# Performance work log

Measured on AMD Instinct MI355X. Metric: run time of the kernel, lower is better.

The kernel has to match this reference:

```python
import jax, jax.numpy as jnp
import numpy as np

D = 1  # dilation


def _unfold3x3(x, d):
    # x: [B, C, H, W] -> [B, H*W, 9, C]; matches torch.nn.Unfold(kernel_size=3,
    # dilation=d, padding=d, stride=1) followed by the module's reshapes.
    B, C, H, W = x.shape
    xp = jnp.pad(x, ((0, 0), (0, 0), (d, d), (d, d)))
    pats = [xp[:, :, i * d:i * d + H, j * d:j * d + W] for i in range(3) for j in range(3)]
    p = jnp.stack(pats, axis=0)  # [9, B, C, H, W], kernel positions row-major (center = 4)
    return p.transpose(1, 3, 4, 0, 2).reshape(B, H * W, 9, C)


def _masked_bn(h, m, gamma, beta, eps=1e-5):
    # BatchNorm1d in training mode applied only to rows selected by bool mask m
    # (the torch code gathers rows, BNs them, scatters back into zeros).
    # Stats are the biased mean/var over the selected rows, per channel.
    axes = tuple(range(h.ndim - 1))
    mf = m[..., None].astype(h.dtype)
    n = jnp.maximum(mf.sum(), 1.0)
    mean = (h * mf).sum(axes) / n
    var = (((h - mean) ** 2 * mf)).sum(axes) / n
    return (h - mean) * jax.lax.rsqrt(var + eps) * gamma + beta


def setup_inputs() -> dict:
    key = jax.random.key(0)
    ks = jax.random.split(key, 8)
    B, H, W = 2, 64, 1024
    Cin, Cout, Cm = 64, 64, 4
    s = 0.1
    x = jax.random.normal(ks[0], (B, Cm + Cin, H, W), jnp.float32)
    mask = (jax.random.uniform(ks[1], (B, 1, H, W)) > 0.3).astype(jnp.float32)
    return {
        "x": x,
        "mask": mask,
        "w1": jax.random.normal(ks[2], (8, Cm), jnp.float32) * s,
        "bn1_g": jnp.ones(8, jnp.float32),
        "bn1_b": jnp.zeros(8, jnp.float32),
        "w2": jax.random.normal(ks[3], (1, 8), jnp.float32) * s,
        "b2": jnp.zeros(1, jnp.float32),
        "g1": jax.random.normal(ks[4], (8, Cm), jnp.float32) * s,
        "gbn1_g": jnp.ones(8, jnp.float32),
        "gbn1_b": jnp.zeros(8, jnp.float32),
        "g2": jax.random.normal(ks[5], (8, 8), jnp.float32) * s,
        "gbn2_g": jnp.ones(8, jnp.float32),
        "gbn2_b": jnp.zeros(8, jnp.float32),
        "w_agg": jax.random.normal(ks[6], (Cout, 72 + Cin), jnp.float32) * s,
        "abn_g": jnp.ones(Cout, jnp.float32),
        "abn_b": jnp.zeros(Cout, jnp.float32),
    }


def reference(x, mask, w1, bn1_g, bn1_b, w2, b2, g1, gbn1_g, gbn1_b, g2, gbn2_g, gbn2_b, w_agg, abn_g, abn_b):
    B, C, H, W = x.shape
    xu = _unfold3x3(x, D)                      # [B, HW, 9, C]
    mu = _unfold3x3(mask, D)[..., 0]           # [B, HW, 9]
    msel = mu > 0                              # valid-neighbor mask
    mp0 = msel[:, :, 4]                        # valid-center mask [B, HW]
    pn = xu[..., :4] - xu[:, :, 4:5, :4]       # relative meta coords [B, HW, 9, 4]
    feats = xu[..., 4:]                        # neighbor features [B, HW, 9, Cin]

    # weight branch (dense compute + mask == torch's gather/scatter)
    h = _masked_bn(pn @ w1.T, msel, bn1_g, bn1_b)
    h = jax.nn.relu(h) @ w2.T + b2             # [B, HW, 9, 1]
    wts = jnp.where(msel, h[..., 0], 0.0)      # zeros at invalid neighbors pre-softmax
    wts = jax.nn.softmax(wts, axis=-1)[..., None]

    fagg = (wts * feats).sum(axis=2)           # [B, HW, Cin]

    # geo branch
    g = jax.nn.relu(_masked_bn(pn @ g1.T, msel, gbn1_g, gbn1_b))
    g = jax.nn.relu(_masked_bn(g @ g2.T, msel, gbn2_g, gbn2_b))
    g = jnp.where(msel[..., None], g, 0.0)
    g = (wts * g).reshape(B, H * W, 72)

    # aggregation over valid centers
    out = jnp.concatenate([fagg, g], axis=-1) @ w_agg.T
    out = jax.nn.relu(_masked_bn(out, mp0, abn_g, abn_b))
    out = jnp.where(mp0[..., None], out, 0.0)  # [B, HW, Cout]
    return out.transpose(0, 2, 1).reshape(B, -1, H, W)  # fold with k=1 == reshape
```

## Files before the change

### kernel.cpp

```cpp
#include <hip/hip_runtime.h>

#define HW_ 65536
#define W_ 1024
#define H_ 64
#define B_ 2
#define C_ 68
#define NPIX 131072
#define EPS 1e-5f

typedef __attribute__((ext_vector_type(8))) short short8;
typedef __attribute__((ext_vector_type(4))) float floatx4;

__device__ __forceinline__ unsigned short f2bf(float f) {
  unsigned u = __float_as_uint(f);
  u += 0x7fffu + ((u >> 16) & 1u);
  return (unsigned short)(u >> 16);
}
__device__ __forceinline__ unsigned pack2(float a, float b) {
  return (unsigned)f2bf(a) | ((unsigned)f2bf(b) << 16);
}
__device__ __forceinline__ float wred(float v) {
  v += __shfl_xor(v, 1);  v += __shfl_xor(v, 2);  v += __shfl_xor(v, 4);
  v += __shfl_xor(v, 8);  v += __shfl_xor(v, 16); v += __shfl_xor(v, 32);
  return v;
}
__device__ __forceinline__ int swz_tile(int bid) {
  return (bid & 7) * 64 + (bid >> 3);
}

__global__ __launch_bounds__(256) void k_stats1(
    const float* __restrict__ x, const float* __restrict__ mask,
    const float* __restrict__ w1, const float* __restrict__ g1,
    float* __restrict__ ws) {
  float acc[34];
#pragma unroll
  for (int i = 0; i < 34; i++) acc[i] = 0.f;

  int p = swz_tile(blockIdx.x) * 256 + threadIdx.x;
  {
    int b = p >> 16, s = p & (HW_ - 1);
    int h = s >> 10, w = s & (W_ - 1);
    const float* xb = x + (size_t)b * C_ * HW_;
    const float* mb = mask + (size_t)b * HW_;
    float xc0 = xb[s], xc1 = xb[HW_ + s], xc2 = xb[2 * HW_ + s], xc3 = xb[3 * HW_ + s];
    acc[33] += (mb[s] > 0.f) ? 1.f : 0.f;
#pragma unroll
    for (int k = 0; k < 9; k++) {
      int di = k / 3 - 1, dj = k % 3 - 1;
      int hh = h + di, ww = w + dj;
      bool inb = ((unsigned)hh < (unsigned)H_) && ((unsigned)ww < (unsigned)W_);
      int ns = hh * W_ + ww;
      float mval = inb ? mb[ns] : 0.f;
      if (mval > 0.f) {
        float pn0 = xb[ns] - xc0;
        float pn1 = xb[HW_ + ns] - xc1;
        float pn2 = xb[2 * HW_ + ns] - xc2;
        float pn3 = xb[3 * HW_ + ns] - xc3;
        acc[32] += 1.f;
#pragma unroll
        for (int o = 0; o < 8; o++) {
          float ta = pn0 * w1[o * 4] + pn1 * w1[o * 4 + 1] + pn2 * w1[o * 4 + 2] + pn3 * w1[o * 4 + 3];
          acc[o] += ta; acc[8 + o] += ta * ta;
          float tg = pn0 * g1[o * 4] + pn1 * g1[o * 4 + 1] + pn2 * g1[o * 4 + 2] + pn3 * g1[o * 4 + 3];
          acc[16 + o] += tg; acc[24 + o] += tg * tg;
        }
      }
    }
  }
  __shared__ float red[4][34];
  int lane = threadIdx.x & 63, wave = threadIdx.x >> 6;
#pragma unroll
  for (int i = 0; i < 34; i++) {
    float r = wred(acc[i]);
    if (lane == 0) red[wave][i] = r;
  }
  __syncthreads();
  if (threadIdx.x < 34)
    atomicAdd(&ws[threadIdx.x],
              red[0][threadIdx.x] + red[1][threadIdx.x] + red[2][threadIdx.x] + red[3][threadIdx.x]);
}

__global__ __launch_bounds__(256) void k_stats2(
    const float* __restrict__ x, const float* __restrict__ mask,
    const float* __restrict__ g1, const float* __restrict__ gbn1_g,
    const float* __restrict__ gbn1_b, const float* __restrict__ g2,
    float* __restrict__ ws) {
  __shared__ float sc[8], sh[8];
  if (threadIdx.x < 8) {
    int o = threadIdx.x;
    float n = fmaxf(ws[32], 1.f);
    float mean = ws[16 + o] / n;
    float var = ws[24 + o] / n - mean * mean;
    float s = gbn1_g[o] * rsqrtf(var + EPS);
    sc[o] = s; sh[o] = gbn1_b[o] - mean * s;
  }
  __syncthreads();

  float acc[16];
#pragma unroll
  for (int i = 0; i < 16; i++) acc[i] = 0.f;

  int p = swz_tile(blockIdx.x) * 256 + threadIdx.x;
  {
    int b = p >> 16, s = p & (HW_ - 1);
    int h = s >> 10, w = s & (W_ - 1);
    const float* xb = x + (size_t)b * C_ * HW_;
    const float* mb = mask + (size_t)b * HW_;
    float xc0 = xb[s], xc1 = xb[HW_ + s], xc2 = xb[2 * HW_ + s], xc3 = xb[3 * HW_ + s];
#pragma unroll
    for (int k = 0; k < 9; k++) {
      int di = k / 3 - 1, dj = k % 3 - 1;
      int hh = h + di, ww = w + dj;
      bool inb = ((unsigned)hh < (unsigned)H_) && ((unsigned)ww < (unsigned)W_);
      int ns = hh * W_ + ww;
      float mval = inb ? mb[ns] : 0.f;
      if (mval > 0.f) {
        float pn0 = xb[ns] - xc0;
        float pn1 = xb[HW_ + ns] - xc1;
        float pn2 = xb[2 * HW_ + ns] - xc2;
        float pn3 = xb[3 * HW_ + ns] - xc3;
        float gb[8];
#pragma unroll
        for (int o = 0; o < 8; o++) {
          float tg = pn0 * g1[o * 4] + pn1 * g1[o * 4 + 1] + pn2 * g1[o * 4 + 2] + pn3 * g1[o * 4 + 3];
          gb[o] = fmaxf(sc[o] * tg + sh[o], 0.f);
        }
#pragma unroll
        for (int j = 0; j < 8; j++) {
          float t2 = 0.f;
#pragma unroll
          for (int o = 0; o < 8; o++) t2 += gb[o] * g2[j * 8 + o];
          acc[j] += t2; acc[8 + j] += t2 * t2;
        }
      }
    }
  }
  __shared__ float red[4][16];
  int lane = threadIdx.x & 63, wave = threadIdx.x >> 6;
#pragma unroll
  for (int i = 0; i < 16; i++) {
    float r = wred(acc[i]);
    if (lane == 0) red[wave][i] = r;
  }
  __syncthreads();
  if (threadIdx.x < 16)
    atomicAdd(&ws[40 + threadIdx.x],
              red[0][threadIdx.x] + red[1][threadIdx.x] + red[2][threadIdx.x] + red[3][threadIdx.x]);
}

__global__ __launch_bounds__(256) void k_fused(
    const float* __restrict__ x, const float* __restrict__ mask,
    const float* __restrict__ w1, const float* __restrict__ bn1_g,
    const float* __restrict__ bn1_b, const float* __restrict__ w2,
    const float* __restrict__ b2, const float* __restrict__ g1,
    const float* __restrict__ gbn1_g, const float* __restrict__ gbn1_b,
    const float* __restrict__ g2, const float* __restrict__ gbn2_g,
    const float* __restrict__ gbn2_b, const float* __restrict__ w_agg,
    const float* __restrict__ ws, float* __restrict__ out_pre,
    float* __restrict__ wsum) {
  __shared__ uint4 vecA[17][256];
  __shared__ float sA[8], hA[8], sG1[8], hG1[8], sG2[8], hG2[8];

  if (threadIdx.x < 24) {
    int o = threadIdx.x & 7;
    float n = fmaxf(ws[32], 1.f);
    float sum, sum2, gma, bta;
    if (threadIdx.x < 8)       { sum = ws[o];      sum2 = ws[8 + o];  gma = bn1_g[o];  bta = bn1_b[o]; }
    else if (threadIdx.x < 16) { sum = ws[16 + o]; sum2 = ws[24 + o]; gma = gbn1_g[o]; bta = gbn1_b[o]; }
    else                       { sum = ws[40 + o]; sum2 = ws[48 + o]; gma = gbn2_g[o]; bta = gbn2_b[o]; }
    float mean = sum / n, var = sum2 / n - mean * mean;
    float s = gma * rsqrtf(var + EPS);
    float sft = bta - mean * s;
    if (threadIdx.x < 8)       { sA[o] = s;  hA[o] = sft; }
    else if (threadIdx.x < 16) { sG1[o] = s; hG1[o] = sft; }
    else                       { sG2[o] = s; hG2[o] = sft; }
  }
  __syncthreads();

  int tile = swz_tile(blockIdx.x);
  int p0 = tile * 256;
  int p = p0 + threadIdx.x;
  int b = p >> 16, s = p & (HW_ - 1);
  int h = s >> 10, w = s & (W_ - 1);
  const float* xb = x + (size_t)b * C_ * HW_;
  const float* mb = mask + (size_t)b * HW_;
  float xc0 = xb[s], xc1 = xb[HW_ + s], xc2 = xb[2 * HW_ + s], xc3 = xb[3 * HW_ + s];
  float b2v = b2[0];

  float ev[9]; int nsv[9]; bool inbv[9], mselv[9];
  float mx = -1e30f;
#pragma unroll
  for (int k = 0; k < 9; k++) {
    int di = k / 3 - 1, dj = k % 3 - 1;
    int hh = h + di, ww = w + dj;
    bool inb = ((unsigned)hh < (unsigned)H_) && ((unsigned)ww < (unsigned)W_);
    int ns = hh * W_ + ww;
    inbv[k] = inb; nsv[k] = ns;
    float mval = inb ? mb[ns] : 0.f;
    bool msel = mval > 0.f;
    mselv[k] = msel;
    float wp = 0.f;
    if (msel) {
      float pn0 = xb[ns] - xc0;
      float pn1 = xb[HW_ + ns] - xc1;
      float pn2 = xb[2 * HW_ + ns] - xc2;
      float pn3 = xb[3 * HW_ + ns] - xc3;
      float accw = 0.f;
#pragma unroll
      for (int o = 0; o < 8; o++) {
        float ta = pn0 * w1[o * 4] + pn1 * w1[o * 4 + 1] + pn2 * w1[o * 4 + 2] + pn3 * w1[o * 4 + 3];
        accw += fmaxf(sA[o] * ta + hA[o], 0.f) * w2[o];
      }
      wp = accw + b2v;
    }
    ev[k] = wp;
    mx = fmaxf(mx, wp);
  }
  float den = 0.f;
#pragma unroll
  for (int k = 0; k < 9; k++) { ev[k] = __expf(ev[k] - mx); den += ev[k]; }
  float inv = 1.f / den;

  float fagg[64];
#pragma unroll
  for (int c = 0; c < 64; c++) fagg[c] = 0.f;

#pragma unroll
  for (int k = 0; k < 9; k++) {
    float wt = ev[k] * inv;
    int ns = nsv[k];
    uint4 pk; pk.x = pk.y = pk.z = pk.w = 0u;
    if (mselv[k]) {
      float pn0 = xb[ns] - xc0;
      float pn1 = xb[HW_ + ns] - xc1;
      float pn2 = xb[2 * HW_ + ns] - xc2;
      float pn3 = xb[3 * HW_ + ns] - xc3;
      float gb[8];
#pragma unroll
      for (int o = 0; o < 8; o++) {
        float tg = pn0 * g1[o * 4] + pn1 * g1[o * 4 + 1] + pn2 * g1[o * 4 + 2] + pn3 * g1[o * 4 + 3];
        gb[o] = fmaxf(sG1[o] * tg + hG1[o], 0.f);
      }
      float gv[8];
#pragma unroll
      for (int j = 0; j < 8; j++) {
        float t2 = 0.f;
#pragma unroll
        for (int o = 0; o < 8; o++) t2 += gb[o] * g2[j * 8 + o];
        float gg = fmaxf(sG2[j] * t2 + hG2[j], 0.f);
        gv[j] = wt * gg;
      }
      pk.x = pack2(gv[0], gv[1]); pk.y = pack2(gv[2], gv[3]);
      pk.z = pack2(gv[4], gv[5]); pk.w = pack2(gv[6], gv[7]);
    }
    vecA[8 + k][threadIdx.x] = pk;
    if (inbv[k]) {
      const float* xf = xb + 4 * HW_ + ns;
#pragma unroll
      for (int c = 0; c < 64; c++) fagg[c] += wt * xf[c * HW_];
    }
  }
#pragma unroll
  for (int c = 0; c < 64; c += 8) {
    uint4 pk;
    pk.x = pack2(fagg[c], fagg[c + 1]);     pk.y = pack2(fagg[c + 2], fagg[c + 3]);
    pk.z = pack2(fagg[c + 4], fagg[c + 5]); pk.w = pack2(fagg[c + 6], fagg[c + 7]);
    vecA[c >> 3][threadIdx.x] = pk;
  }
  __syncthreads();

  int lane = threadIdx.x & 63, wave = threadIdx.x >> 6;
  int q = lane >> 4, r = lane & 15;

  short8 Bf[4][5];
#pragma unroll
  for (int nt = 0; nt < 4; nt++) {
    int n = nt * 16 + r;
#pragma unroll
    for (int ks = 0; ks < 5; ks++) {
      int k0 = ks * 32 + q * 8;
      uint4 pk; pk.x = pk.y = pk.z = pk.w = 0u;
      if (k0 < 136) {
        float4 f0 = *reinterpret_cast<const float4*>(w_agg + n * 136 + k0);
        float4 f1 = *reinterpret_cast<const float4*>(w_agg + n * 136 + k0 + 4);
        pk.x = pack2(f0.x, f0.y); pk.y = pack2(f0.z, f0.w);
        pk.z = pack2(f1.x, f1.y); pk.w = pack2(f1.z, f1.w);
      }
      Bf[nt][ks] = *reinterpret_cast<short8*>(&pk);
    }
  }

  floatx4 acc[4][4];
#pragma unroll
  for (int m = 0; m < 4; m++)
#pragma unroll
    for (int nt = 0; nt < 4; nt++) acc[m][nt] = (floatx4){0.f, 0.f, 0.f, 0.f};

#pragma unroll
  for (int m = 0; m < 4; m++) {
    int mt = wave * 4 + m;
    int pix = mt * 16 + r;
    short8 Af[5];
#pragma unroll
    for (int ks = 0; ks < 5; ks++) {
      int chunk = ks * 4 + q;
      if (chunk < 17)
        Af[ks] = *reinterpret_cast<const short8*>(&vecA[chunk][pix]);
      else
        Af[ks] = (short8){0, 0, 0, 0, 0, 0, 0, 0};
    }
#pragma unroll
    for (int nt = 0; nt < 4; nt++)
#pragma unroll
      for (int ks = 0; ks < 5; ks++)
        acc[m][nt] = __builtin_amdgcn_mfma_f32_16x16x32_bf16(Af[ks], Bf[nt][ks], acc[m][nt], 0, 0, 0);
  }

  float aS[4] = {0.f, 0.f, 0.f, 0.f}, aQ[4] = {0.f, 0.f, 0.f, 0.f};
  int s0 = p0 & (HW_ - 1);
#pragma unroll
  for (int m = 0; m < 4; m++) {
    int mt = wave * 4 + m;
    int srow = s0 + mt * 16 + q * 4;
    float4 mv = *reinterpret_cast<const float4*>(mb + srow);
    float m0 = (mv.x > 0.f) ? 1.f : 0.f, m1 = (mv.y > 0.f) ? 1.f : 0.f;
    float m2 = (mv.z > 0.f) ? 1.f : 0.f, m3 = (mv.w > 0.f) ? 1.f : 0.f;
#pragma unroll
    for (int nt = 0; nt < 4; nt++) {
      int ch = nt * 16 + r;
      float4 ov;
      ov.x = acc[m][nt][0]; ov.y = acc[m][nt][1];
      ov.z = acc[m][nt][2]; ov.w = acc[m][nt][3];
      aS[nt] += ov.x * m0 + ov.y * m1 + ov.z * m2 + ov.w * m3;
      aQ[nt] += ov.x * ov.x * m0 + ov.y * ov.y * m1 + ov.z * ov.z * m2 + ov.w * ov.w * m3;
      *reinterpret_cast<float4*>(out_pre + ((size_t)(b * 64 + ch)) * HW_ + srow) = ov;
    }
  }

  __syncthreads();
  float* rS = (float*)&vecA[0][0];
  float* rQ = rS + 256;
#pragma unroll
  for (int nt = 0; nt < 4; nt++) {
    float v1 = aS[nt], v2 = aQ[nt];
    v1 += __shfl_xor(v1, 16); v1 += __shfl_xor(v1, 32);
    v2 += __shfl_xor(v2, 16); v2 += __shfl_xor(v2, 32);
    if (lane < 16) { rS[wave * 64 + nt * 16 + lane] = v1; rQ[wave * 64 + nt * 16 + lane] = v2; }
  }
  __syncthreads();
  if (threadIdx.x < 64) {
    atomicAdd(&wsum[64 + threadIdx.x],
              rS[threadIdx.x] + rS[64 + threadIdx.x] + rS[128 + threadIdx.x] + rS[192 + threadIdx.x]);
    atomicAdd(&wsum[128 + threadIdx.x],
              rQ[threadIdx.x] + rQ[64 + threadIdx.x] + rQ[128 + threadIdx.x] + rQ[192 + threadIdx.x]);
  }
}

__global__ __launch_bounds__(256) void k_final(
    const float* __restrict__ out_pre, const float* __restrict__ mask,
    const float* __restrict__ abn_g, const float* __restrict__ abn_b,
    const float* __restrict__ ws, float* __restrict__ out) {
  __shared__ float sc[64], sh[64];
  if (threadIdx.x < 64) {
    int c = threadIdx.x;
    float n0 = fmaxf(ws[33], 1.f);
    float mean = ws[64 + c] / n0;
    float var = ws[128 + c] / n0 - mean * mean;
    float s = abn_g[c] * rsqrtf(var + EPS);
    sc[c] = s; sh[c] = abn_b[c] - mean * s;
  }
  __syncthreads();
  int i4 = (blockIdx.x * 256 + threadIdx.x) * 4;
  if (i4 >= B_ * 64 * HW_) return;
  int c = (i4 >> 16) & 63;
  int b = i4 >> 22;
  int s = i4 & (HW_ - 1);
  float4 v = *reinterpret_cast<const float4*>(out_pre + i4);
  float4 m = *reinterpret_cast<const float4*>(mask + (size_t)b * HW_ + s);
  float4 o;
  o.x = (m.x > 0.f) ? fmaxf(v.x * sc[c] + sh[c], 0.f) : 0.f;
  o.y = (m.y > 0.f) ? fmaxf(v.y * sc[c] + sh[c], 0.f) : 0.f;
  o.z = (m.z > 0.f) ? fmaxf(v.z * sc[c] + sh[c], 0.f) : 0.f;
  o.w = (m.w > 0.f) ? fmaxf(v.w * sc[c] + sh[c], 0.f) : 0.f;
  *reinterpret_cast<float4*>(out + i4) = o;
}

extern "C" void kernel_launch(void* const* d_in, const int* in_sizes, int n_in,
                              void* d_out, int out_size, void* d_ws, size_t ws_size,
                              hipStream_t stream) {
  const float* x      = (const float*)d_in[0];
  const float* mask   = (const float*)d_in[1];
  const float* w1     = (const float*)d_in[2];
  const float* bn1_g  = (const float*)d_in[3];
  const float* bn1_b  = (const float*)d_in[4];
  const float* w2     = (const float*)d_in[5];
  const float* b2     = (const float*)d_in[6];
  const float* g1     = (const float*)d_in[7];
  const float* gbn1_g = (const float*)d_in[8];
  const float* gbn1_b = (const float*)d_in[9];
  const float* g2     = (const float*)d_in[10];
  const float* gbn2_g = (const float*)d_in[11];
  const float* gbn2_b = (const float*)d_in[12];
  const float* w_agg  = (const float*)d_in[13];
  const float* abn_g  = (const float*)d_in[14];
  const float* abn_b  = (const float*)d_in[15];
  float* out = (float*)d_out;

  size_t need = 1024 + (size_t)NPIX * 64 * 4;
  if (ws_size < need) return;

  float* wsf = (float*)d_ws;
  float* out_pre = (float*)((char*)d_ws + 1024);

  hipMemsetAsync(d_ws, 0, 1024, stream);
  k_stats1<<<512, 256, 0, stream>>>(x, mask, w1, g1, wsf);
  k_stats2<<<512, 256, 0, stream>>>(x, mask, g1, gbn1_g, gbn1_b, g2, wsf);
  k_fused<<<512, 256, 0, stream>>>(x, mask, w1, bn1_g, bn1_b, w2, b2, g1,
                                   gbn1_g, gbn1_b, g2, gbn2_g, gbn2_b, w_agg,
                                   wsf, out_pre, wsf);
  k_final<<<8192, 256, 0, stream>>>(out_pre, mask, abn_g, abn_b, wsf, out);
}
```

Before: 224.5 us.

## Fuse all stages into one persistent kernel with software grid barriers

Merges the two statistics kernels, the fused compute kernel and the final BN kernel into a single 512-block launch that synchronises BatchNorm statistics through atomic-counter grid barriers. Neighbor meta deltas are kept in registers across phases, and the final BN/ReLU is applied straight from the MFMA accumulators. This drops the 32 MB out_pre intermediate write and re-read plus three extra launches. It relies on all 512 blocks being co-resident (launch_bounds 256,2 on 256 CUs). The barrier gives up after a spin cap, which could silently yield wrong statistics, and the larger live register state may cause spills.

```diff
diff --git a/kernel.cpp b/kernel.cpp
--- a/kernel.cpp
+++ b/kernel.cpp
@@ -6,6 +6,7 @@
 #define B_ 2
 #define C_ 68
 #define NPIX 131072
+#define NBLK 512
 #define EPS 1e-5f
 
 typedef __attribute__((ext_vector_type(8))) short short8;
@@ -27,128 +28,33 @@
 __device__ __forceinline__ int swz_tile(int bid) {
   return (bid & 7) * 64 + (bid >> 3);
 }
-
-__global__ __launch_bounds__(256) void k_stats1(
-    const float* __restrict__ x, const float* __restrict__ mask,
-    const float* __restrict__ w1, const float* __restrict__ g1,
-    float* __restrict__ ws) {
-  float acc[34];
-#pragma unroll
-  for (int i = 0; i < 34; i++) acc[i] = 0.f;
-
-  int p = swz_tile(blockIdx.x) * 256 + threadIdx.x;
-  {
-    int b = p >> 16, s = p & (HW_ - 1);
-    int h = s >> 10, w = s & (W_ - 1);
-    const float* xb = x + (size_t)b * C_ * HW_;
-    const float* mb = mask + (size_t)b * HW_;
-    float xc0 = xb[s], xc1 = xb[HW_ + s], xc2 = xb[2 * HW_ + s], xc3 = xb[3 * HW_ + s];
-    acc[33] += (mb[s] > 0.f) ? 1.f : 0.f;
-#pragma unroll
-    for (int k = 0; k < 9; k++) {
-      int di = k / 3 - 1, dj = k % 3 - 1;
-      int hh = h + di, ww = w + dj;
-      bool inb = ((unsigned)hh < (unsigned)H_) && ((unsigned)ww < (unsigned)W_);
-      int ns = hh * W_ + ww;
-      float mval = inb ? mb[ns] : 0.f;
-      if (mval > 0.f) {
-        float pn0 = xb[ns] - xc0;
-        float pn1 = xb[HW_ + ns] - xc1;
-        float pn2 = xb[2 * HW_ + ns] - xc2;
-        float pn3 = xb[3 * HW_ + ns] - xc3;
-        acc[32] += 1.f;
-#pragma unroll
-        for (int o = 0; o < 8; o++) {
-          float ta = pn0 * w1[o * 4] + pn1 * w1[o * 4 + 1] + pn2 * w1[o * 4 + 2] + pn3 * w1[o * 4 + 3];
-          acc[o] += ta; acc[8 + o] += ta * ta;
-          float tg = pn0 * g1[o * 4] + pn1 * g1[o * 4 + 1] + pn2 * g1[o * 4 + 2] + pn3 * g1[o * 4 + 3];
-          acc[16 + o] += tg; acc[24 + o] += tg * tg;
-        }
-      }
-    }
-  }
-  __shared__ float red[4][34];
-  int lane = threadIdx.x & 63, wave = threadIdx.x >> 6;
-#pragma unroll
-  for (int i = 0; i < 34; i++) {
-    float r = wred(acc[i]);
-    if (lane == 0) red[wave][i] = r;
-  }
-  __syncthreads();
-  if (threadIdx.x < 34)
-    atomicAdd(&ws[threadIdx.x],
-              red[0][threadIdx.x] + red[1][threadIdx.x] + red[2][threadIdx.x] + red[3][threadIdx.x]);
-}
-
-__global__ __launch_bounds__(256) void k_stats2(
-    const float* __restrict__ x, const float* __restrict__ mask,
-    const float* __restrict__ g1, const float* __restrict__ gbn1_g,
-    const float* __restrict__ gbn1_b, const float* __restrict__ g2,
-    float* __restrict__ ws) {
-  __shared__ float sc[8], sh[8];
-  if (threadIdx.x < 8) {
-    int o = threadIdx.x;
-    float n = fmaxf(ws[32], 1.f);
-    float mean = ws[16 + o] / n;
-    float var = ws[24 + o] / n - mean * mean;
-    float s = gbn1_g[o] * rsqrtf(var + EPS);
-    sc[o] = s; sh[o] = gbn1_b[o] - mean * s;
-  }
-  __syncthreads();
-
-  float acc[16];
-#pragma unroll
-  for (int i = 0; i < 16; i++) acc[i] = 0.f;
-
-  int p = swz_tile(blockIdx.x) * 256 + threadIdx.x;
-  {
-    int b = p >> 16, s = p & (HW_ - 1);
-    int h = s >> 10, w = s & (W_ - 1);
-    const float* xb = x + (size_t)b * C_ * HW_;
-    const float* mb = mask + (size_t)b * HW_;
-    float xc0 = xb[s], xc1 = xb[HW_ + s], xc2 = xb[2 * HW_ + s], xc3 = xb[3 * HW_ + s];
-#pragma unroll
-    for (int k = 0; k < 9; k++) {
-      int di = k / 3 - 1, dj = k % 3 - 1;
-      int hh = h + di, ww = w + dj;
-      bool inb = ((unsigned)hh < (unsigned)H_) && ((unsigned)ww < (unsigned)W_);
-      int ns = hh * W_ + ww;
-      float mval = inb ? mb[ns] : 0.f;
-      if (mval > 0.f) {
-        float pn0 = xb[ns] - xc0;
-        float pn1 = xb[HW_ + ns] - xc1;
-        float pn2 = xb[2 * HW_ + ns] - xc2;
-        float pn3 = xb[3 * HW_ + ns] - xc3;
-        float gb[8];
-#pragma unroll
-        for (int o = 0; o < 8; o++) {
-          float tg = pn0 * g1[o * 4] + pn1 * g1[o * 4 + 1] + pn2 * g1[o * 4 + 2] + pn3 * g1[o * 4 + 3];
-          gb[o] = fmaxf(sc[o] * tg + sh[o], 0.f);
-        }
-#pragma unroll
-        for (int j = 0; j < 8; j++) {
-          float t2 = 0.f;
-#pragma unroll
-          for (int o = 0; o < 8; o++) t2 += gb[o] * g2[j * 8 + o];
-          acc[j] += t2; acc[8 + j] += t2 * t2;
-        }
-      }
-    }
-  }
-  __shared__ float red[4][16];
-  int lane = threadIdx.x & 63, wave = threadIdx.x >> 6;
-#pragma unroll
-  for (int i = 0; i < 16; i++) {
-    float r = wred(acc[i]);
-    if (lane == 0) red[wave][i] = r;
-  }
-  __syncthreads();
-  if (threadIdx.x < 16)
-    atomicAdd(&ws[40 + threadIdx.x],
-              red[0][threadIdx.x] + red[1][threadIdx.x] + red[2][threadIdx.x] + red[3][threadIdx.x]);
-}
-
-__global__ __launch_bounds__(256) void k_fused(
+__device__ __forceinline__ float wsld(const float* p) {
+  return __hip_atomic_load(p, __ATOMIC_RELAXED, __HIP_MEMORY_SCOPE_AGENT);
+}
+
+__device__ __forceinline__ void gridbar(unsigned* bar) {
+  __syncthreads();
+  if (threadIdx.x == 0) {
+    __threadfence();
+    unsigned gen = __hip_atomic_load(&bar[1], __ATOMIC_RELAXED, __HIP_MEMORY_SCOPE_AGENT);
+    unsigned arrived =
+        __hip_atomic_fetch_add(&bar[0], 1u, __ATOMIC_ACQ_REL, __HIP_MEMORY_SCOPE_AGENT);
+    if (arrived == NBLK - 1) {
+      __hip_atomic_store(&bar[0], 0u, __ATOMIC_RELAXED, __HIP_MEMORY_SCOPE_AGENT);
+      __hip_atomic_store(&bar[1], gen + 1u, __ATOMIC_RELEASE, __HIP_MEMORY_SCOPE_AGENT);
+    } else {
+      long long spins = 0;
+      while (__hip_atomic_load(&bar[1], __ATOMIC_ACQUIRE, __HIP_MEMORY_SCOPE_AGENT) == gen) {
+        if (++spins > (1LL << 22)) break;
+        __builtin_amdgcn_s_sleep(8);
+      }
+    }
+    __threadfence();
+  }
+  __syncthreads();
+}
+
+__global__ __launch_bounds__(256, 2) void k_all(
     const float* __restrict__ x, const float* __restrict__ mask,
     const float* __restrict__ w1, const float* __restrict__ bn1_g,
     const float* __restrict__ bn1_b, const float* __restrict__ w2,
@@ -156,59 +62,152 @@
     const float* __restrict__ gbn1_g, const float* __restrict__ gbn1_b,
     const float* __restrict__ g2, const float* __restrict__ gbn2_g,
     const float* __restrict__ gbn2_b, const float* __restrict__ w_agg,
-    const float* __restrict__ ws, float* __restrict__ out_pre,
-    float* __restrict__ wsum) {
+    const float* __restrict__ abn_g, const float* __restrict__ abn_b,
+    float* __restrict__ ws, float* __restrict__ out) {
+  unsigned* bar = (unsigned*)(ws + 248);
+
   __shared__ uint4 vecA[17][256];
+  __shared__ float red[4][34];
   __shared__ float sA[8], hA[8], sG1[8], hG1[8], sG2[8], hG2[8];
-
-  if (threadIdx.x < 24) {
-    int o = threadIdx.x & 7;
-    float n = fmaxf(ws[32], 1.f);
-    float sum, sum2, gma, bta;
-    if (threadIdx.x < 8)       { sum = ws[o];      sum2 = ws[8 + o];  gma = bn1_g[o];  bta = bn1_b[o]; }
-    else if (threadIdx.x < 16) { sum = ws[16 + o]; sum2 = ws[24 + o]; gma = gbn1_g[o]; bta = gbn1_b[o]; }
-    else                       { sum = ws[40 + o]; sum2 = ws[48 + o]; gma = gbn2_g[o]; bta = gbn2_b[o]; }
-    float mean = sum / n, var = sum2 / n - mean * mean;
-    float s = gma * rsqrtf(var + EPS);
-    float sft = bta - mean * s;
-    if (threadIdx.x < 8)       { sA[o] = s;  hA[o] = sft; }
-    else if (threadIdx.x < 16) { sG1[o] = s; hG1[o] = sft; }
-    else                       { sG2[o] = s; hG2[o] = sft; }
-  }
-  __syncthreads();
+  __shared__ float scD[64], shD[64];
 
   int tile = swz_tile(blockIdx.x);
   int p0 = tile * 256;
-  int p = p0 + threadIdx.x;
+  int p = p0 + (int)threadIdx.x;
   int b = p >> 16, s = p & (HW_ - 1);
   int h = s >> 10, w = s & (W_ - 1);
   const float* xb = x + (size_t)b * C_ * HW_;
   const float* mb = mask + (size_t)b * HW_;
+  int lane = threadIdx.x & 63, wave = threadIdx.x >> 6;
+  int q = lane >> 4, r = lane & 15;
+
   float xc0 = xb[s], xc1 = xb[HW_ + s], xc2 = xb[2 * HW_ + s], xc3 = xb[3 * HW_ + s];
-  float b2v = b2[0];
-
-  float ev[9]; int nsv[9]; bool inbv[9], mselv[9];
-  float mx = -1e30f;
+
+  float pn[9][4];
+  int nsv[9];
+  unsigned mbits = 0u, ibits = 0u;
+  float cntk = 0.f;
 #pragma unroll
   for (int k = 0; k < 9; k++) {
     int di = k / 3 - 1, dj = k % 3 - 1;
     int hh = h + di, ww = w + dj;
     bool inb = ((unsigned)hh < (unsigned)H_) && ((unsigned)ww < (unsigned)W_);
     int ns = hh * W_ + ww;
-    inbv[k] = inb; nsv[k] = ns;
+    nsv[k] = ns;
+    pn[k][0] = 0.f; pn[k][1] = 0.f; pn[k][2] = 0.f; pn[k][3] = 0.f;
+    if (inb) ibits |= (1u << k);
     float mval = inb ? mb[ns] : 0.f;
-    bool msel = mval > 0.f;
-    mselv[k] = msel;
+    if (mval > 0.f) {
+      mbits |= (1u << k);
+      cntk += 1.f;
+      pn[k][0] = xb[ns] - xc0;
+      pn[k][1] = xb[HW_ + ns] - xc1;
+      pn[k][2] = xb[2 * HW_ + ns] - xc2;
+      pn[k][3] = xb[3 * HW_ + ns] - xc3;
+    }
+  }
+
+  {
+    float acc[34];
+#pragma unroll
+    for (int i = 0; i < 34; i++) acc[i] = 0.f;
+    acc[32] = cntk;
+    acc[33] = (mbits & 16u) ? 1.f : 0.f;
+#pragma unroll
+    for (int k = 0; k < 9; k++) {
+      if ((mbits >> k) & 1u) {
+#pragma unroll
+        for (int o = 0; o < 8; o++) {
+          float ta = pn[k][0] * w1[o * 4] + pn[k][1] * w1[o * 4 + 1] +
+                     pn[k][2] * w1[o * 4 + 2] + pn[k][3] * w1[o * 4 + 3];
+          acc[o] += ta; acc[8 + o] += ta * ta;
+          float tg = pn[k][0] * g1[o * 4] + pn[k][1] * g1[o * 4 + 1] +
+                     pn[k][2] * g1[o * 4 + 2] + pn[k][3] * g1[o * 4 + 3];
+          acc[16 + o] += tg; acc[24 + o] += tg * tg;
+        }
+      }
+    }
+#pragma unroll
+    for (int i = 0; i < 34; i++) {
+      float rv = wred(acc[i]);
+      if (lane == 0) red[wave][i] = rv;
+    }
+    __syncthreads();
+    if (threadIdx.x < 34)
+      atomicAdd(&ws[threadIdx.x],
+                red[0][threadIdx.x] + red[1][threadIdx.x] + red[2][threadIdx.x] + red[3][threadIdx.x]);
+  }
+  gridbar(bar);
+
+  if (threadIdx.x < 16) {
+    int o = threadIdx.x & 7;
+    float n = fmaxf(wsld(&ws[32]), 1.f);
+    float sum, sum2, gma, bta;
+    if (threadIdx.x < 8) { sum = wsld(&ws[o]);      sum2 = wsld(&ws[8 + o]);  gma = bn1_g[o];  bta = bn1_b[o]; }
+    else                 { sum = wsld(&ws[16 + o]); sum2 = wsld(&ws[24 + o]); gma = gbn1_g[o]; bta = gbn1_b[o]; }
+    float mean = sum / n, var = sum2 / n - mean * mean;
+    float sc_ = gma * rsqrtf(var + EPS);
+    float sh_ = bta - mean * sc_;
+    if (threadIdx.x < 8) { sA[o] = sc_;  hA[o] = sh_; }
+    else                 { sG1[o] = sc_; hG1[o] = sh_; }
+  }
+  __syncthreads();
+  {
+    float acc2[16];
+#pragma unroll
+    for (int i = 0; i < 16; i++) acc2[i] = 0.f;
+#pragma unroll
+    for (int k = 0; k < 9; k++) {
+      if ((mbits >> k) & 1u) {
+        float gb[8];
+#pragma unroll
+        for (int o = 0; o < 8; o++) {
+          float tg = pn[k][0] * g1[o * 4] + pn[k][1] * g1[o * 4 + 1] +
+                     pn[k][2] * g1[o * 4 + 2] + pn[k][3] * g1[o * 4 + 3];
+          gb[o] = fmaxf(sG1[o] * tg + hG1[o], 0.f);
+        }
+#pragma unroll
+        for (int j = 0; j < 8; j++) {
+          float t2 = 0.f;
+#pragma unroll
+          for (int o = 0; o < 8; o++) t2 += gb[o] * g2[j * 8 + o];
+          acc2[j] += t2; acc2[8 + j] += t2 * t2;
+        }
+      }
+    }
+#pragma unroll
+    for (int i = 0; i < 16; i++) {
+      float rv = wred(acc2[i]);
+      if (lane == 0) red[wave][i] = rv;
+    }
+    __syncthreads();
+    if (threadIdx.x < 16)
+      atomicAdd(&ws[40 + threadIdx.x],
+                red[0][threadIdx.x] + red[1][threadIdx.x] + red[2][threadIdx.x] + red[3][threadIdx.x]);
+  }
+  gridbar(bar);
+
+  if (threadIdx.x < 8) {
+    int o = threadIdx.x;
+    float n = fmaxf(wsld(&ws[32]), 1.f);
+    float mean = wsld(&ws[40 + o]) / n, var = wsld(&ws[48 + o]) / n - mean * mean;
+    float sc_ = gbn2_g[o] * rsqrtf(var + EPS);
+    sG2[o] = sc_; hG2[o] = gbn2_b[o] - mean * sc_;
+  }
+  __syncthreads();
+
+  float b2v = b2[0];
+  float ev[9];
+  float mx = -1e30f;
+#pragma unroll
+  for (int k = 0; k < 9; k++) {
     float wp = 0.f;
-    if (msel) {
-      float pn0 = xb[ns] - xc0;
-      float pn1 = xb[HW_ + ns] - xc1;
-      float pn2 = xb[2 * HW_ + ns] - xc2;
-      float pn3 = xb[3 * HW_ + ns] - xc3;
+    if ((mbits >> k) & 1u) {
       float accw = 0.f;
 #pragma unroll
       for (int o = 0; o < 8; o++) {
-        float ta = pn0 * w1[o * 4] + pn1 * w1[o * 4 + 1] + pn2 * w1[o * 4 + 2] + pn3 * w1[o * 4 + 3];
+        float ta = pn[k][0] * w1[o * 4] + pn[k][1] * w1[o * 4 + 1] +
+                   pn[k][2] * w1[o * 4 + 2] + pn[k][3] * w1[o * 4 + 3];
         accw += fmaxf(sA[o] * ta + hA[o], 0.f) * w2[o];
       }
       wp = accw + b2v;
@@ -221,24 +220,16 @@
   for (int k = 0; k < 9; k++) { ev[k] = __expf(ev[k] - mx); den += ev[k]; }
   float inv = 1.f / den;
 
-  float fagg[64];
-#pragma unroll
-  for (int c = 0; c < 64; c++) fagg[c] = 0.f;
-
 #pragma unroll
   for (int k = 0; k < 9; k++) {
     float wt = ev[k] * inv;
-    int ns = nsv[k];
     uint4 pk; pk.x = pk.y = pk.z = pk.w = 0u;
-    if (mselv[k]) {
-      float pn0 = xb[ns] - xc0;
-      float pn1 = xb[HW_ + ns] - xc1;
-      float pn2 = xb[2 * HW_ + ns] - xc2;
-      float pn3 = xb[3 * HW_ + ns] - xc3;
+    if ((mbits >> k) & 1u) {
       float gb[8];
 #pragma unroll
       for (int o = 0; o < 8; o++) {
-        float tg = pn0 * g1[o * 4] + pn1 * g1[o * 4 + 1] + pn2 * g1[o * 4 + 2] + pn3 * g1[o * 4 + 3];
+        float tg = pn[k][0] * g1[o * 4] + pn[k][1] * g1[o * 4 + 1] +
+                   pn[k][2] * g1[o * 4 + 2] + pn[k][3] * g1[o * 4 + 3];
         gb[o] = fmaxf(sG1[o] * tg + hG1[o], 0.f);
       }
       float gv[8];
@@ -254,8 +245,16 @@
       pk.z = pack2(gv[4], gv[5]); pk.w = pack2(gv[6], gv[7]);
     }
     vecA[8 + k][threadIdx.x] = pk;
-    if (inbv[k]) {
-      const float* xf = xb + 4 * HW_ + ns;
+  }
+
+  float fagg[64];
+#pragma unroll
+  for (int c = 0; c < 64; c++) fagg[c] = 0.f;
+#pragma unroll
+  for (int k = 0; k < 9; k++) {
+    if ((ibits >> k) & 1u) {
+      float wt = ev[k] * inv;
+      const float* xf = xb + 4 * HW_ + nsv[k];
 #pragma unroll
       for (int c = 0; c < 64; c++) fagg[c] += wt * xf[c * HW_];
     }
@@ -268,9 +267,6 @@
     vecA[c >> 3][threadIdx.x] = pk;
   }
   __syncthreads();
-
-  int lane = threadIdx.x & 63, wave = threadIdx.x >> 6;
-  int q = lane >> 4, r = lane & 15;
 
   short8 Bf[4][5];
 #pragma unroll
@@ -327,13 +323,9 @@
     float m2 = (mv.z > 0.f) ? 1.f : 0.f, m3 = (mv.w > 0.f) ? 1.f : 0.f;
 #pragma unroll
     for (int nt = 0; nt < 4; nt++) {
-      int ch = nt * 16 + r;
-      float4 ov;
-      ov.x = acc[m][nt][0]; ov.y = acc[m][nt][1];
-      ov.z = acc[m][nt][2]; ov.w = acc[m][nt][3];
-      aS[nt] += ov.x * m0 + ov.y * m1 + ov.z * m2 + ov.w * m3;
-      aQ[nt] += ov.x * ov.x * m0 + ov.y * ov.y * m1 + ov.z * ov.z * m2 + ov.w * ov.w * m3;
-      *reinterpret_cast<float4*>(out_pre + ((size_t)(b * 64 + ch)) * HW_ + srow) = ov;
+      aS[nt] += acc[m][nt][0] * m0 + acc[m][nt][1] * m1 + acc[m][nt][2] * m2 + acc[m][nt][3] * m3;
+      aQ[nt] += acc[m][nt][0] * acc[m][nt][0] * m0 + acc[m][nt][1] * acc[m][nt][1] * m1 +
+                acc[m][nt][2] * acc[m][nt][2] * m2 + acc[m][nt][3] * acc[m][nt][3] * m3;
     }
   }
 
@@ -349,40 +341,39 @@
   }
   __syncthreads();
   if (threadIdx.x < 64) {
-    atomicAdd(&wsum[64 + threadIdx.x],
+    atomicAdd(&ws[64 + threadIdx.x],
               rS[threadIdx.x] + rS[64 + threadIdx.x] + rS[128 + threadIdx.x] + rS[192 + threadIdx.x]);
-    atomicAdd(&wsum[128 + threadIdx.x],
+    atomicAdd(&ws[128 + threadIdx.x],
               rQ[threadIdx.x] + rQ[64 + threadIdx.x] + rQ[128 + threadIdx.x] + rQ[192 + threadIdx.x]);
   }
-}
-
-__global__ __launch_bounds__(256) void k_final(
-    const float* __restrict__ out_pre, const float* __restrict__ mask,
-    const float* __restrict__ abn_g, const float* __restrict__ abn_b,
-    const float* __restrict__ ws, float* __restrict__ out) {
-  __shared__ float sc[64], sh[64];
+  gridbar(bar);
+
   if (threadIdx.x < 64) {
     int c = threadIdx.x;
-    float n0 = fmaxf(ws[33], 1.f);
-    float mean = ws[64 + c] / n0;
-    float var = ws[128 + c] / n0 - mean * mean;
-    float s = abn_g[c] * rsqrtf(var + EPS);
-    sc[c] = s; sh[c] = abn_b[c] - mean * s;
-  }
-  __syncthreads();
-  int i4 = (blockIdx.x * 256 + threadIdx.x) * 4;
-  if (i4 >= B_ * 64 * HW_) return;
-  int c = (i4 >> 16) & 63;
-  int b = i4 >> 22;
-  int s = i4 & (HW_ - 1);
-  float4 v = *reinterpret_cast<const float4*>(out_pre + i4);
-  float4 m = *reinterpret_cast<const float4*>(mask + (size_t)b * HW_ + s);
-  float4 o;
-  o.x = (m.x > 0.f) ? fmaxf(v.x * sc[c] + sh[c], 0.f) : 0.f;
-  o.y = (m.y > 0.f) ? fmaxf(v.y * sc[c] + sh[c], 0.f) : 0.f;
-  o.z = (m.z > 0.f) ? fmaxf(v.z * sc[c] + sh[c], 0.f) : 0.f;
-  o.w = (m.w > 0.f) ? fmaxf(v.w * sc[c] + sh[c], 0.f) : 0.f;
-  *reinterpret_cast<float4*>(out + i4) = o;
+    float n0 = fmaxf(wsld(&ws[33]), 1.f);
+    float mean = wsld(&ws[64 + c]) / n0;
+    float var = wsld(&ws[128 + c]) / n0 - mean * mean;
+    float sc_ = abn_g[c] * rsqrtf(var + EPS);
+    scD[c] = sc_; shD[c] = abn_b[c] - mean * sc_;
+  }
+  __syncthreads();
+#pragma unroll
+  for (int m = 0; m < 4; m++) {
+    int mt = wave * 4 + m;
+    int srow = s0 + mt * 16 + q * 4;
+    float4 mv = *reinterpret_cast<const float4*>(mb + srow);
+#pragma unroll
+    for (int nt = 0; nt < 4; nt++) {
+      int ch = nt * 16 + r;
+      float sc_ = scD[ch], sh_ = shD[ch];
+      float4 ov;
+      ov.x = (mv.x > 0.f) ? fmaxf(acc[m][nt][0] * sc_ + sh_, 0.f) : 0.f;
+      ov.y = (mv.y > 0.f) ? fmaxf(acc[m][nt][1] * sc_ + sh_, 0.f) : 0.f;
+      ov.z = (mv.z > 0.f) ? fmaxf(acc[m][nt][2] * sc_ + sh_, 0.f) : 0.f;
+      ov.w = (mv.w > 0.f) ? fmaxf(acc[m][nt][3] * sc_ + sh_, 0.f) : 0.f;
+      *reinterpret_cast<float4*>(out + ((size_t)(b * 64 + ch)) * HW_ + srow) = ov;
+    }
+  }
 }
 
 extern "C" void kernel_launch(void* const* d_in, const int* in_sizes, int n_in,
@@ -406,17 +397,12 @@
   const float* abn_b  = (const float*)d_in[15];
   float* out = (float*)d_out;
 
-  size_t need = 1024 + (size_t)NPIX * 64 * 4;
-  if (ws_size < need) return;
-
+  if (ws_size < 1024) return;
   float* wsf = (float*)d_ws;
-  float* out_pre = (float*)((char*)d_ws + 1024);
 
   hipMemsetAsync(d_ws, 0, 1024, stream);
-  k_stats1<<<512, 256, 0, stream>>>(x, mask, w1, g1, wsf);
-  k_stats2<<<512, 256, 0, stream>>>(x, mask, g1, gbn1_g, gbn1_b, g2, wsf);
-  k_fused<<<512, 256, 0, stream>>>(x, mask, w1, bn1_g, bn1_b, w2, b2, g1,
-                                   gbn1_g, gbn1_b, g2, gbn2_g, gbn2_b, w_agg,
-                                   wsf, out_pre, wsf);
-  k_final<<<8192, 256, 0, stream>>>(out_pre, mask, abn_g, abn_b, wsf, out);
-}
+
+  k_all<<<NBLK, 256, 0, stream>>>(x, mask, w1, bn1_g, bn1_b, w2, b2, g1,
+                                  gbn1_g, gbn1_b, g2, gbn2_g, gbn2_b, w_agg,
+                                  abn_g, abn_b, wsf, out);
+}
```

Measured after the change: 411.0 us. 83.1% more time.

## Merge two stats kernels into one with a software grid barrier

Applied to the files above, without the earlier changes.

Combines the two BatchNorm statistics passes into a single persistent kernel of 512 blocks. Each thread keeps its 9 neighbor relative coordinates and validity bits in registers, and a spin-based grid barrier separates the first-stage stats from the second-stage stats. This removes one kernel launch and the second pass's re-read of x and mask. The barrier needs all 512 blocks to be resident at once and has a spin-count timeout that could silently break synchronization. Keeping the coordinates in registers also raises register pressure.

```diff
diff --git a/kernel.cpp b/kernel.cpp
--- a/kernel.cpp
+++ b/kernel.cpp
@@ -6,6 +6,7 @@
 #define B_ 2
 #define C_ 68
 #define NPIX 131072
+#define NBLK 512
 #define EPS 1e-5f
 
 typedef __attribute__((ext_vector_type(8))) short short8;
@@ -27,125 +28,145 @@
 __device__ __forceinline__ int swz_tile(int bid) {
   return (bid & 7) * 64 + (bid >> 3);
 }
-
-__global__ __launch_bounds__(256) void k_stats1(
+__device__ __forceinline__ float wsld(const float* p) {
+  return __hip_atomic_load(p, __ATOMIC_RELAXED, __HIP_MEMORY_SCOPE_AGENT);
+}
+
+__device__ __forceinline__ void gridbar(unsigned* bar) {
+  __syncthreads();
+  if (threadIdx.x == 0) {
+    __threadfence();
+    unsigned gen = __hip_atomic_load(&bar[1], __ATOMIC_RELAXED, __HIP_MEMORY_SCOPE_AGENT);
+    unsigned arrived =
+        __hip_atomic_fetch_add(&bar[0], 1u, __ATOMIC_ACQ_REL, __HIP_MEMORY_SCOPE_AGENT);
+    if (arrived == NBLK - 1) {
+      __hip_atomic_store(&bar[0], 0u, __ATOMIC_RELAXED, __HIP_MEMORY_SCOPE_AGENT);
+      __hip_atomic_store(&bar[1], gen + 1u, __ATOMIC_RELEASE, __HIP_MEMORY_SCOPE_AGENT);
+    } else {
+      long long spins = 0;
+      while (__hip_atomic_load(&bar[1], __ATOMIC_ACQUIRE, __HIP_MEMORY_SCOPE_AGENT) == gen) {
+        if (++spins > (1LL << 22)) break;
+        __builtin_amdgcn_s_sleep(8);
+      }
+    }
+    __threadfence();
+  }
+  __syncthreads();
+}
+
+__global__ __launch_bounds__(256, 2) void k_stats(
     const float* __restrict__ x, const float* __restrict__ mask,
     const float* __restrict__ w1, const float* __restrict__ g1,
-    float* __restrict__ ws) {
-  float acc[34];
-#pragma unroll
-  for (int i = 0; i < 34; i++) acc[i] = 0.f;
-
-  int p = swz_tile(blockIdx.x) * 256 + threadIdx.x;
+    const float* __restrict__ gbn1_g, const float* __restrict__ gbn1_b,
+    const float* __restrict__ g2, float* __restrict__ ws) {
+  unsigned* bar = (unsigned*)(ws + 248);
+  __shared__ float red[4][34];
+  __shared__ float sG1[8], hG1[8];
+
+  int p = swz_tile(blockIdx.x) * 256 + (int)threadIdx.x;
+  int b = p >> 16, s = p & (HW_ - 1);
+  int h = s >> 10, w = s & (W_ - 1);
+  const float* xb = x + (size_t)b * C_ * HW_;
+  const float* mb = mask + (size_t)b * HW_;
+  int lane = threadIdx.x & 63, wave = threadIdx.x >> 6;
+
+  float xc0 = xb[s], xc1 = xb[HW_ + s], xc2 = xb[2 * HW_ + s], xc3 = xb[3 * HW_ + s];
+
+  float pn[9][4];
+  unsigned mbits = 0u;
+  float cntk = 0.f;
+#pragma unroll
+  for (int k = 0; k < 9; k++) {
+    int di = k / 3 - 1, dj = k % 3 - 1;
+    int hh = h + di, ww = w + dj;
+    bool inb = ((unsigned)hh < (unsigned)H_) && ((unsigned)ww < (unsigned)W_);
+    int ns = hh * W_ + ww;
+    pn[k][0] = 0.f; pn[k][1] = 0.f; pn[k][2] = 0.f; pn[k][3] = 0.f;
+    float mval = inb ? mb[ns] : 0.f;
+    if (mval > 0.f) {
+      mbits |= (1u << k);
+      cntk += 1.f;
+      pn[k][0] = xb[ns] - xc0;
+      pn[k][1] = xb[HW_ + ns] - xc1;
+      pn[k][2] = xb[2 * HW_ + ns] - xc2;
+      pn[k][3] = xb[3 * HW_ + ns] - xc3;
+    }
+  }
+
   {
-    int b = p >> 16, s = p & (HW_ - 1);
-    int h = s >> 10, w = s & (W_ - 1);
-    const float* xb = x + (size_t)b * C_ * HW_;
-    const float* mb = mask + (size_t)b * HW_;
-    float xc0 = xb[s], xc1 = xb[HW_ + s], xc2 = xb[2 * HW_ + s], xc3 = xb[3 * HW_ + s];
-    acc[33] += (mb[s] > 0.f) ? 1.f : 0.f;
+    float acc[34];
+#pragma unroll
+    for (int i = 0; i < 34; i++) acc[i] = 0.f;
+    acc[32] = cntk;
+    acc[33] = (mbits & 16u) ? 1.f : 0.f;
 #pragma unroll
     for (int k = 0; k < 9; k++) {
-      int di = k / 3 - 1, dj = k % 3 - 1;
-      int hh = h + di, ww = w + dj;
-      bool inb = ((unsigned)hh < (unsigned)H_) && ((unsigned)ww < (unsigned)W_);
-      int ns = hh * W_ + ww;
-      float mval = inb ? mb[ns] : 0.f;
-      if (mval > 0.f) {
-        float pn0 = xb[ns] - xc0;
-        float pn1 = xb[HW_ + ns] - xc1;
-        float pn2 = xb[2 * HW_ + ns] - xc2;
-        float pn3 = xb[3 * HW_ + ns] - xc3;
-        acc[32] += 1.f;
+      if ((mbits >> k) & 1u) {
 #pragma unroll
         for (int o = 0; o < 8; o++) {
-          float ta = pn0 * w1[o * 4] + pn1 * w1[o * 4 + 1] + pn2 * w1[o * 4 + 2] + pn3 * w1[o * 4 + 3];
+          float ta = pn[k][0] * w1[o * 4] + pn[k][1] * w1[o * 4 + 1] +
+                     pn[k][2] * w1[o * 4 + 2] + pn[k][3] * w1[o * 4 + 3];
           acc[o] += ta; acc[8 + o] += ta * ta;
-          float tg = pn0 * g1[o * 4] + pn1 * g1[o * 4 + 1] + pn2 * g1[o * 4 + 2] + pn3 * g1[o * 4 + 3];
+          float tg = pn[k][0] * g1[o * 4] + pn[k][1] * g1[o * 4 + 1] +
+                     pn[k][2] * g1[o * 4 + 2] + pn[k][3] * g1[o * 4 + 3];
           acc[16 + o] += tg; acc[24 + o] += tg * tg;
         }
       }
     }
-  }
-  __shared__ float red[4][34];
-  int lane = threadIdx.x & 63, wave = threadIdx.x >> 6;
-#pragma unroll
-  for (int i = 0; i < 34; i++) {
-    float r = wred(acc[i]);
-    if (lane == 0) red[wave][i] = r;
-  }
-  __syncthreads();
-  if (threadIdx.x < 34)
-    atomicAdd(&ws[threadIdx.x],
-              red[0][threadIdx.x] + red[1][threadIdx.x] + red[2][threadIdx.x] + red[3][threadIdx.x]);
-}
-
-__global__ __launch_bounds__(256) void k_stats2(
-    const float* __restrict__ x, const float* __restrict__ mask,
-    const float* __restrict__ g1, const float* __restrict__ gbn1_g,
-    const float* __restrict__ gbn1_b, const float* __restrict__ g2,
-    float* __restrict__ ws) {
-  __shared__ float sc[8], sh[8];
+#pragma unroll
+    for (int i = 0; i < 34; i++) {
+      float rv = wred(acc[i]);
+      if (lane == 0) red[wave][i] = rv;
+    }
+    __syncthreads();
+    if (threadIdx.x < 34)
+      atomicAdd(&ws[threadIdx.x],
+                red[0][threadIdx.x] + red[1][threadIdx.x] + red[2][threadIdx.x] + red[3][threadIdx.x]);
+  }
+  gridbar(bar);
+
   if (threadIdx.x < 8) {
     int o = threadIdx.x;
-    float n = fmaxf(ws[32], 1.f);
-    float mean = ws[16 + o] / n;
-    float var = ws[24 + o] / n - mean * mean;
-    float s = gbn1_g[o] * rsqrtf(var + EPS);
-    sc[o] = s; sh[o] = gbn1_b[o] - mean * s;
-  }
-  __syncthreads();
-
-  float acc[16];
-#pragma unroll
-  for (int i = 0; i < 16; i++) acc[i] = 0.f;
-
-  int p = swz_tile(blockIdx.x) * 256 + threadIdx.x;
+    float n = fmaxf(wsld(&ws[32]), 1.f);
+    float mean = wsld(&ws[16 + o]) / n;
+    float var = wsld(&ws[24 + o]) / n - mean * mean;
+    float sc_ = gbn1_g[o] * rsqrtf(var + EPS);
+    sG1[o] = sc_; hG1[o] = gbn1_b[o] - mean * sc_;
+  }
+  __syncthreads();
   {
-    int b = p >> 16, s = p & (HW_ - 1);
-    int h = s >> 10, w = s & (W_ - 1);
-    const float* xb = x + (size_t)b * C_ * HW_;
-    const float* mb = mask + (size_t)b * HW_;
-    float xc0 = xb[s], xc1 = xb[HW_ + s], xc2 = xb[2 * HW_ + s], xc3 = xb[3 * HW_ + s];
+    float acc2[16];
+#pragma unroll
+    for (int i = 0; i < 16; i++) acc2[i] = 0.f;
 #pragma unroll
     for (int k = 0; k < 9; k++) {
-      int di = k / 3 - 1, dj = k % 3 - 1;
-      int hh = h + di, ww = w + dj;
-      bool inb = ((unsigned)hh < (unsigned)H_) && ((unsigned)ww < (unsigned)W_);
-      int ns = hh * W_ + ww;
-      float mval = inb ? mb[ns] : 0.f;
-      if (mval > 0.f) {
-        float pn0 = xb[ns] - xc0;
-        float pn1 = xb[HW_ + ns] - xc1;
-        float pn2 = xb[2 * HW_ + ns] - xc2;
-        float pn3 = xb[3 * HW_ + ns] - xc3;
+      if ((mbits >> k) & 1u) {
         float gb[8];
 #pragma unroll
         for (int o = 0; o < 8; o++) {
-          float tg = pn0 * g1[o * 4] + pn1 * g1[o * 4 + 1] + pn2 * g1[o * 4 + 2] + pn3 * g1[o * 4 + 3];
-          gb[o] = fmaxf(sc[o] * tg + sh[o], 0.f);
+          float tg = pn[k][0] * g1[o * 4] + pn[k][1] * g1[o * 4 + 1] +
+                     pn[k][2] * g1[o * 4 + 2] + pn[k][3] * g1[o * 4 + 3];
+          gb[o] = fmaxf(sG1[o] * tg + hG1[o], 0.f);
         }
 #pragma unroll
         for (int j = 0; j < 8; j++) {
           float t2 = 0.f;
 #pragma unroll
           for (int o = 0; o < 8; o++) t2 += gb[o] * g2[j * 8 + o];
-          acc[j] += t2; acc[8 + j] += t2 * t2;
+          acc2[j] += t2; acc2[8 + j] += t2 * t2;
         }
       }
     }
-  }
-  __shared__ float red[4][16];
-  int lane = threadIdx.x & 63, wave = threadIdx.x >> 6;
-#pragma unroll
-  for (int i = 0; i < 16; i++) {
-    float r = wred(acc[i]);
-    if (lane == 0) red[wave][i] = r;
-  }
-  __syncthreads();
-  if (threadIdx.x < 16)
-    atomicAdd(&ws[40 + threadIdx.x],
-              red[0][threadIdx.x] + red[1][threadIdx.x] + red[2][threadIdx.x] + red[3][threadIdx.x]);
+#pragma unroll
+    for (int i = 0; i < 16; i++) {
+      float rv = wred(acc2[i]);
+      if (lane == 0) red[wave][i] = rv;
+    }
+    __syncthreads();
+    if (threadIdx.x < 16)
+      atomicAdd(&ws[40 + threadIdx.x],
+                red[0][threadIdx.x] + red[1][threadIdx.x] + red[2][threadIdx.x] + red[3][threadIdx.x]);
+  }
 }
 
 __global__ __launch_bounds__(256) void k_fused(
@@ -413,10 +434,9 @@
   float* out_pre = (float*)((char*)d_ws + 1024);
 
   hipMemsetAsync(d_ws, 0, 1024, stream);
-  k_stats1<<<512, 256, 0, stream>>>(x, mask, w1, g1, wsf);
-  k_stats2<<<512, 256, 0, stream>>>(x, mask, g1, gbn1_g, gbn1_b, g2, wsf);
-  k_fused<<<512, 256, 0, stream>>>(x, mask, w1, bn1_g, bn1_b, w2, b2, g1,
-                                   gbn1_g, gbn1_b, g2, gbn2_g, gbn2_b, w_agg,
-                                   wsf, out_pre, wsf);
+  k_stats<<<NBLK, 256, 0, stream>>>(x, mask, w1, g1, gbn1_g, gbn1_b, g2, wsf);
+  k_fused<<<NBLK, 256, 0, stream>>>(x, mask, w1, bn1_g, bn1_b, w2, b2, g1,
+                                    gbn1_g, gbn1_b, g2, gbn2_g, gbn2_b, w_agg,
+                                    wsf, out_pre, wsf);
   k_final<<<8192, 256, 0, stream>>>(out_pre, mask, abn_g, abn_b, wsf, out);
 }
```

Result: slower. 272.3 us (+21.3%).
